# Kernel optimization log

Hardware: AMD Instinct MI355X
Metric: run time of the kernel (lower is better)

Reference implementation:

```python
import jax, jax.numpy as jnp
import numpy as np

N = 50000
E = 800000
NODE_F = 5
MAP_F = 32
EDGE_F = 4
HID = 64
RNN = 20
RNN_E = 8
LAT = 32
OUT = 4


def setup_inputs() -> dict:
    key = jax.random.key(0)
    ks = iter(jax.random.split(key, 40))
    def rn(shape, scale=0.1):
        return jax.random.normal(next(ks), shape, dtype=jnp.float32) * scale
    inp = {
        "x": rn((N, NODE_F), 1.0),
        "u": rn((N, MAP_F), 1.0),
        "edge_index": jax.random.randint(next(ks), (2, E), 0, N, dtype=jnp.int32),
        "edge_attr": rn((E, EDGE_F), 1.0),
        "h_node_h": rn((N, RNN), 1.0),
        "h_node_c": rn((N, RNN), 1.0),
        "h_edge_h": rn((N, RNN_E), 1.0),
        "h_edge_c": rn((N, RNN_E), 1.0),
        # node-history LSTM (input = node_features + map_encoding_size = 37)
        "W_ih_n": rn((4 * RNN, NODE_F + MAP_F)), "W_hh_n": rn((4 * RNN, RNN)),
        "b_ih_n": jnp.zeros((4 * RNN,), jnp.float32), "b_hh_n": jnp.zeros((4 * RNN,), jnp.float32),
        # edge-history LSTM (input = latent_edge_features)
        "W_ih_e": rn((4 * RNN_E, LAT)), "W_hh_e": rn((4 * RNN_E, RNN_E)),
        "b_ih_e": jnp.zeros((4 * RNN_E,), jnp.float32), "b_hh_e": jnp.zeros((4 * RNN_E,), jnp.float32),
        # message edge MLP: in = 2*37 + 4 = 78 -> 64 -> 32
        "We1": rn((2 * (NODE_F + MAP_F) + EDGE_F, HID)), "be1": jnp.zeros((HID,), jnp.float32),
        "We2": rn((HID, LAT)), "be2": jnp.zeros((LAT,), jnp.float32),
        # GN_out edge MLP: in = 2*(rnn_size + rnn_edge_size) + 4 = 60 -> 64 -> 32
        "Wo1": rn((2 * (RNN + RNN_E) + EDGE_F, HID)), "bo1": jnp.zeros((HID,), jnp.float32),
        "Wo2": rn((HID, LAT)), "bo2": jnp.zeros((LAT,), jnp.float32),
        # GN_out node MLP: in = (rnn_size + rnn_edge_size) + latent = 60 -> 64 -> 4
        "Wn1": rn((RNN + RNN_E + LAT, HID)), "bn1": jnp.zeros((HID,), jnp.float32),
        "Wn2": rn((HID, OUT)), "bn2": jnp.zeros((OUT,), jnp.float32),
    }
    return inp


def _lstm_step(xin, h, c, Wih, Whh, bih, bhh):
    # torch gate order: i, f, g, o
    g = xin @ Wih.T + h @ Whh.T + bih + bhh
    i, f, gg, o = jnp.split(g, 4, axis=-1)
    c_new = jax.nn.sigmoid(f) * c + jax.nn.sigmoid(i) * jnp.tanh(gg)
    h_new = jax.nn.sigmoid(o) * jnp.tanh(c_new)
    return h_new, c_new


def _segment_mean(vals, idx, n):
    s = jax.ops.segment_sum(vals, idx, num_segments=n)
    cnt = jax.ops.segment_sum(jnp.ones((vals.shape[0], 1), vals.dtype), idx, num_segments=n)
    return s / jnp.maximum(cnt, 1.0)


def _edge_mlp(src, dst, edge_attr, W1, b1, W2, b2):
    h = jnp.concatenate([src, dst, edge_attr], axis=-1)
    return jax.nn.relu(h @ W1 + b1) @ W2 + b2


def reference(x, u, edge_index, edge_attr, h_node_h, h_node_c, h_edge_h, h_edge_c,
              W_ih_n, W_hh_n, b_ih_n, b_hh_n, W_ih_e, W_hh_e, b_ih_e, b_hh_e,
              We1, be1, We2, be2, Wo1, bo1, Wo2, bo2, Wn1, bn1, Wn2, bn2):
    n = x.shape[0]
    xu = jnp.concatenate([x, u], axis=-1)  # [N, 37]
    # node history RNN step
    node_hist, node_c = _lstm_step(xu, h_node_h, h_node_c, W_ih_n, W_hh_n, b_ih_n, b_hh_n)
    # message GN: gather -> edge MLP
    row, col = edge_index[0], edge_index[1]
    messages = _edge_mlp(xu[row], xu[col], edge_attr, We1, be1, We2, be2)  # [E, 32]
    # edge history RNN: aggregate messages per receiving node, then LSTM step
    agg_msg = _segment_mean(messages, col, n)  # [N, 32]
    edge_hist, edge_c = _lstm_step(agg_msg, h_edge_h, h_edge_c, W_ih_e, W_hh_e, b_ih_e, b_hh_e)
    # output GN block
    full = jnp.concatenate([node_hist, edge_hist], axis=-1)  # [N, 28]
    e2 = _edge_mlp(full[row], full[col], edge_attr, Wo1, bo1, Wo2, bo2)  # [E, 32]
    agg2 = _segment_mean(e2, col, n)  # [N, 32]
    node_in = jnp.concatenate([full, agg2], axis=-1)  # [N, 60]
    out = jax.nn.relu(node_in @ Wn1 + bn1) @ Wn2 + bn2  # [N, 4]
    return (out, node_hist, node_c, edge_hist, edge_c)
```

## Files before the change

### kernel.cpp

```cpp
#include <hip/hip_runtime.h>
#include <math.h>

#define NN 50000
#define EE 800000
#define SBLK ((NN + 255) / 256)

typedef short bf16x8 __attribute__((ext_vector_type(8)));
typedef float f32x4 __attribute__((ext_vector_type(4)));
typedef unsigned short ushort_t;
#define MFMA16(a, b, c) __builtin_amdgcn_mfma_f32_16x16x32_bf16(a, b, c, 0, 0, 0)

__device__ __forceinline__ float sigmoidf_(float x) { return 1.0f / (1.0f + __expf(-x)); }

__device__ __forceinline__ unsigned short f2bf(float f) {
    unsigned u = __builtin_bit_cast(unsigned, f);
    u += 0x7FFFu + ((u >> 16) & 1u);
    return (unsigned short)(u >> 16);
}
__device__ __forceinline__ float bf2f(unsigned short v) {
    unsigned u = (unsigned)v << 16;
    return __builtin_bit_cast(float, u);
}
__device__ __forceinline__ unsigned pk2(float a, float b) {
    return ((unsigned)f2bf(b) << 16) | (unsigned)f2bf(a);
}

__global__ __launch_bounds__(256) void node_lstm_k(
    const float* __restrict__ x, const float* __restrict__ u,
    const float* __restrict__ h0, const float* __restrict__ c0,
    const float* __restrict__ Wih, const float* __restrict__ Whh,
    const float* __restrict__ bih, const float* __restrict__ bhh,
    ushort_t* __restrict__ xu16, float* __restrict__ h_out, float* __restrict__ c_out)
{
    __shared__ float sWih[80 * 37];
    __shared__ float sWhh[80 * 20];
    __shared__ float sb[80];
    for (int i = threadIdx.x; i < 80 * 37; i += 256) sWih[i] = Wih[i];
    for (int i = threadIdx.x; i < 80 * 20; i += 256) sWhh[i] = Whh[i];
    if (threadIdx.x < 80) sb[threadIdx.x] = bih[threadIdx.x] + bhh[threadIdx.x];
    __syncthreads();
    int n = blockIdx.x * 256 + threadIdx.x;
    if (n >= NN) return;

    float xu[40];
#pragma unroll
    for (int k = 0; k < 5; k++) xu[k] = x[n * 5 + k];
#pragma unroll
    for (int k = 0; k < 32; k++) xu[5 + k] = u[n * 32 + k];
    xu[37] = 0.f; xu[38] = 0.f; xu[39] = 0.f;

    {
        unsigned w[20];
#pragma unroll
        for (int k = 0; k < 20; k++) w[k] = pk2(xu[2 * k], xu[2 * k + 1]);
        uint4* dst = (uint4*)(xu16 + (size_t)n * 40);
#pragma unroll
        for (int q = 0; q < 5; q++)
            dst[q] = make_uint4(w[q * 4], w[q * 4 + 1], w[q * 4 + 2], w[q * 4 + 3]);
    }

    float h[20];
#pragma unroll
    for (int k = 0; k < 20; k++) h[k] = h0[n * 20 + k];

#pragma unroll 1
    for (int r = 0; r < 20; r++) {
        float gi = sb[r], gf = sb[20 + r], gg = sb[40 + r], go = sb[60 + r];
#pragma unroll
        for (int k = 0; k < 37; k++) {
            float v = xu[k];
            gi = fmaf(v, sWih[r * 37 + k], gi);
            gf = fmaf(v, sWih[(20 + r) * 37 + k], gf);
            gg = fmaf(v, sWih[(40 + r) * 37 + k], gg);
            go = fmaf(v, sWih[(60 + r) * 37 + k], go);
        }
#pragma unroll
        for (int k = 0; k < 20; k++) {
            float v = h[k];
            gi = fmaf(v, sWhh[r * 20 + k], gi);
            gf = fmaf(v, sWhh[(20 + r) * 20 + k], gf);
            gg = fmaf(v, sWhh[(40 + r) * 20 + k], gg);
            go = fmaf(v, sWhh[(60 + r) * 20 + k], go);
        }
        float cr = c0[n * 20 + r];
        float cn = sigmoidf_(gf) * cr + sigmoidf_(gi) * tanhf(gg);
        float hn = sigmoidf_(go) * tanhf(cn);
        h_out[n * 20 + r] = hn;
        c_out[n * 20 + r] = cn;
    }
}

__global__ __launch_bounds__(256) void csr_count_k(const int* __restrict__ col,
                                                   int* __restrict__ count)
{
    int e = blockIdx.x * 256 + threadIdx.x;
    if (e < EE) atomicAdd(&count[col[e]], 1);
}

__global__ __launch_bounds__(256) void scan1_k(const int* __restrict__ count,
                                               int* __restrict__ bsum)
{
    __shared__ int red[256];
    int t = threadIdx.x;
    int i = blockIdx.x * 256 + t;
    red[t] = (i < NN) ? count[i] : 0;
    __syncthreads();
#pragma unroll
    for (int d = 128; d > 0; d >>= 1) {
        if (t < d) red[t] += red[t + d];
        __syncthreads();
    }
    if (t == 0) bsum[blockIdx.x] = red[0];
}

__global__ __launch_bounds__(256) void scan2_k(const int* __restrict__ bsum,
                                               int* __restrict__ bpre)
{
    __shared__ int s[256];
    int t = threadIdx.x;
    int v = (t < SBLK) ? bsum[t] : 0;
    s[t] = v;
    __syncthreads();
#pragma unroll
    for (int d = 1; d < 256; d <<= 1) {
        int w = (t >= d) ? s[t - d] : 0;
        __syncthreads();
        s[t] += w;
        __syncthreads();
    }
    if (t < SBLK) bpre[t] = s[t] - v;
}

__global__ __launch_bounds__(256) void scan3_k(const int* __restrict__ count,
                                               const int* __restrict__ bpre,
                                               int* __restrict__ offset,
                                               float* __restrict__ cntf)
{
    __shared__ int s[256];
    int t = threadIdx.x;
    int i = blockIdx.x * 256 + t;
    int v = (i < NN) ? count[i] : 0;
    s[t] = v;
    __syncthreads();
#pragma unroll
    for (int d = 1; d < 256; d <<= 1) {
        int w = (t >= d) ? s[t - d] : 0;
        __syncthreads();
        s[t] += w;
        __syncthreads();
    }
    if (i < NN) {
        offset[i] = bpre[blockIdx.x] + s[t] - v;
        cntf[i] = (float)v;
    }
}

__global__ __launch_bounds__(256) void csr_fill3_k(const int* __restrict__ row,
                                                   const int* __restrict__ col,
                                                   const float* __restrict__ eattr,
                                                   const int* __restrict__ offset,
                                                   int* __restrict__ cursor,
                                                   int* __restrict__ rowp,
                                                   int* __restrict__ colp,
                                                   ushort_t* __restrict__ eap)
{
    int e = blockIdx.x * 256 + threadIdx.x;
    if (e >= EE) return;
    int c = col[e];
    int pos = atomicAdd(&cursor[c], 1);
    int slot = offset[c] + pos;
    rowp[slot] = row[e];
    colp[slot] = c;
    float4 ev = *(const float4*)&eattr[(size_t)e * 4];
    uint2 pk = make_uint2(pk2(ev.x, ev.y), pk2(ev.z, ev.w));
    *(uint2*)&eap[(size_t)slot * 4] = pk;
}

template <int F, int STRIDE, int INK>
__global__ __launch_bounds__(256, 4) void edge_mlp_fused_k(
    const ushort_t* __restrict__ feat,
    const int* __restrict__ rowp, const int* __restrict__ colp,
    const ushort_t* __restrict__ eap,
    const int* __restrict__ offset, const int* __restrict__ count,
    const float* __restrict__ W1, const float* __restrict__ b1,
    const float* __restrict__ W2, const float* __restrict__ b2,
    float* __restrict__ agg)
{
    constexpr int S1 = INK / 32;
    constexpr int W1ST = INK + 8;
    constexpr int C1ST = 72;
    constexpr int ABYTES = (64 * W1ST + 32 * C1ST + 4 * 32 * C1ST) * 2;
    constexpr int BBYTES = 32 * 257 * 4;
    constexpr int UBYTES = (ABYTES > BBYTES) ? ABYTES : BBYTES;

    __shared__ __align__(16) char ldsu[UBYTES];
    __shared__ int colLds[256];
    __shared__ unsigned char segStartA[256];
    __shared__ short segEndA[256];
    __shared__ int segCnt;

    ushort_t* sW1 = (ushort_t*)ldsu;
    ushort_t* sW2 = sW1 + 64 * W1ST;
    ushort_t* sC1 = sW2 + 32 * C1ST;
    float*    msgT = (float*)ldsu;

    const int tid = threadIdx.x;
    const int B0 = blockIdx.x * 256;
    if (tid == 0) segCnt = 0;
    colLds[tid] = colp[B0 + tid];

    for (int i = tid; i < 64 * INK; i += 256) {
        int nk = i >> 6, n = i & 63;
        int kp = 0; bool z = false;
        if (F == 37) {
            if (nk < 37) kp = nk;
            else if (nk < 40) z = true;
            else if (nk < 77) kp = nk - 3;
            else if (nk < 80) z = true;
            else if (nk < 84) kp = nk - 6;
            else z = true;
        } else {
            if (nk < 28) kp = nk;
            else if (nk < 32) z = true;
            else kp = nk - 4;
        }
        sW1[n * W1ST + nk] = z ? (ushort_t)0 : f2bf(W1[kp * 64 + n]);
    }
    for (int i = tid; i < 64 * 32; i += 256) {
        int k = i >> 5, n = i & 31;
        sW2[n * C1ST + k] = f2bf(W2[k * 32 + n]);
    }
    __syncthreads();

    {
        bool isStart = (tid == 0) || (colLds[tid] != colLds[tid - 1]);
        if (isStart) {
            int node = colLds[tid];
            int off = offset[node], cn = count[node];
            int e = off + cn - B0; if (e > 256) e = 256;
            bool fullseg = (off >= B0) && (off + cn <= B0 + 256);
            int j = atomicAdd(&segCnt, 1);
            segStartA[j] = (unsigned char)tid;
            segEndA[j] = (short)(fullseg ? -e : e);
        }
    }

    const int wave = tid >> 6, lane = tid & 63;
    const int lr = lane & 15, jb = lane >> 4;
    const size_t slotBase = (size_t)B0 + (size_t)wave * 64;
    const float4* b1v = (const float4*)b1;
    ushort_t* myC1 = sC1 + wave * 32 * C1ST;
    const float bb2_0 = b2[lr], bb2_1 = b2[16 + lr];

    f32x4 acc2a[2][2][2];

#pragma unroll
    for (int half = 0; half < 2; half++) {
        bf16x8 xf[2][S1];
#pragma unroll
        for (int ne2 = 0; ne2 < 2; ne2++) {
            size_t slot = slotBase + (size_t)(half * 2 + ne2) * 16 + lr;
            const ushort_t* xr = feat + (size_t)rowp[slot] * STRIDE;
            const ushort_t* xc = feat + (size_t)colLds[slot - B0] * STRIDE;
            const ushort_t* ea = eap + slot * 4;
            xf[ne2][0] = *(const bf16x8*)(xr + jb * 8);
            if (F == 37) {
                const ushort_t* p1 = (jb == 0) ? (xr + 32) : (xc + (jb - 1) * 8);
                xf[ne2][1] = *(const bf16x8*)p1;
                const ushort_t* p2 = (jb == 0) ? (xc + 24) : ((jb == 1) ? (xc + 32) : ea);
                bf16x8 v = *(const bf16x8*)p2;
                if (jb >= 2) { v[4] = 0; v[5] = 0; v[6] = 0; v[7] = 0; }
                if (jb == 3) { v[0] = 0; v[1] = 0; v[2] = 0; v[3] = 0; }
                xf[ne2][2] = v;
            } else {
                const ushort_t* pl = (jb < 3) ? (xc + jb * 8) : (xc + 24);
                uint2 lo = *(const uint2*)pl;
                const ushort_t* ph = (jb < 3) ? (pl + 4) : ea;
                uint2 hi = *(const uint2*)ph;
                uint4 cc = make_uint4(lo.x, lo.y, hi.x, hi.y);
                xf[ne2][1] = __builtin_bit_cast(bf16x8, cc);
            }
        }

        f32x4 acc1[4][2];
#pragma unroll
        for (int mh = 0; mh < 4; mh++) {
            float4 bv = b1v[mh * 4 + jb];
            f32x4 bi = {bv.x, bv.y, bv.z, bv.w};
            acc1[mh][0] = bi; acc1[mh][1] = bi;
        }
#pragma unroll
        for (int s = 0; s < S1; s++) {
#pragma unroll
            for (int mh = 0; mh < 4; mh++) {
                bf16x8 wf = *(const bf16x8*)&sW1[(mh * 16 + lr) * W1ST + s * 32 + jb * 8];
                acc1[mh][0] = MFMA16(wf, xf[0][s], acc1[mh][0]);
                acc1[mh][1] = MFMA16(wf, xf[1][s], acc1[mh][1]);
            }
        }

#pragma unroll
        for (int mh = 0; mh < 4; mh++) {
#pragma unroll
            for (int ne2 = 0; ne2 < 2; ne2++) {
                f32x4 a = acc1[mh][ne2];
                unsigned w0 = pk2(fmaxf(a[0], 0.f), fmaxf(a[1], 0.f));
                unsigned w1 = pk2(fmaxf(a[2], 0.f), fmaxf(a[3], 0.f));
                *(uint2*)&myC1[(ne2 * 16 + lr) * C1ST + mh * 16 + jb * 4] = make_uint2(w0, w1);
            }
        }

#pragma unroll
        for (int m = 0; m < 2; m++) {
            acc2a[half][m][0] = f32x4{bb2_0, bb2_0, bb2_0, bb2_0};
            acc2a[half][m][1] = f32x4{bb2_1, bb2_1, bb2_1, bb2_1};
        }
#pragma unroll
        for (int s2 = 0; s2 < 2; s2++) {
            bf16x8 w2f0 = *(const bf16x8*)&sW2[lr * C1ST + s2 * 32 + jb * 8];
            bf16x8 w2f1 = *(const bf16x8*)&sW2[(16 + lr) * C1ST + s2 * 32 + jb * 8];
#pragma unroll
            for (int m = 0; m < 2; m++) {
                bf16x8 a2 = *(const bf16x8*)&myC1[(m * 16 + lr) * C1ST + s2 * 32 + jb * 8];
                acc2a[half][m][0] = MFMA16(a2, w2f0, acc2a[half][m][0]);
                acc2a[half][m][1] = MFMA16(a2, w2f1, acc2a[half][m][1]);
            }
        }
    }

    __syncthreads();
#pragma unroll
    for (int half = 0; half < 2; half++) {
#pragma unroll
        for (int m = 0; m < 2; m++) {
            int row = wave * 64 + (half * 2 + m) * 16 + jb * 4;
#pragma unroll
            for (int n = 0; n < 2; n++) {
                f32x4 a = acc2a[half][m][n];
                float* dst = &msgT[(size_t)(n * 16 + lr) * 257 + row];
                dst[0] = a[0]; dst[1] = a[1]; dst[2] = a[2]; dst[3] = a[3];
            }
        }
    }
    __syncthreads();

    {
        int f = lane & 31;
        int h = lane >> 5;
        const float* mrow = msgT + (size_t)f * 257;
        int nseg = segCnt;
        for (int j = wave; j < nseg; j += 4) {
            int s = segStartA[j];
            int ev = segEndA[j];
            bool fullseg = ev < 0;
            int e = fullseg ? -ev : ev;
            int node = colLds[s];
            float sum = 0.f;
            for (int i = s + h; i < e; i += 2) sum += mrow[i];
            sum += __shfl_xor(sum, 32);
            if (lane < 32) {
                float* dst = &agg[(size_t)node * 32 + f];
                if (fullseg) *dst = sum;
                else atomicAdd(dst, sum);
            }
        }
    }
}

__global__ __launch_bounds__(256) void edge_lstm_k(
    const float* __restrict__ agg, const float* __restrict__ cnt,
    const float* __restrict__ h0, const float* __restrict__ c0,
    const float* __restrict__ Wih, const float* __restrict__ Whh,
    const float* __restrict__ bih, const float* __restrict__ bhh,
    const float* __restrict__ node_h,
    float* __restrict__ h_out, float* __restrict__ c_out, ushort_t* __restrict__ full16)
{
    __shared__ float sWih[32 * 32];
    __shared__ float sWhh[32 * 8];
    __shared__ float sb[32];
    for (int i = threadIdx.x; i < 32 * 32; i += 256) sWih[i] = Wih[i];
    for (int i = threadIdx.x; i < 32 * 8; i += 256) sWhh[i] = Whh[i];
    if (threadIdx.x < 32) sb[threadIdx.x] = bih[threadIdx.x] + bhh[threadIdx.x];
    __syncthreads();
    int n = blockIdx.x * 256 + threadIdx.x;
    if (n >= NN) return;

    float inv = 1.0f / fmaxf(cnt[n], 1.0f);
    float msg[32];
#pragma unroll
    for (int k = 0; k < 32; k++) msg[k] = agg[(size_t)n * 32 + k] * inv;
    float h[8];
#pragma unroll
    for (int k = 0; k < 8; k++) h[k] = h0[n * 8 + k];

    float fl[32];
#pragma unroll
    for (int k = 0; k < 20; k++) fl[k] = node_h[n * 20 + k];
    fl[28] = 0.f; fl[29] = 0.f; fl[30] = 0.f; fl[31] = 0.f;

#pragma unroll
    for (int r = 0; r < 8; r++) {
        float gi = sb[r], gf = sb[8 + r], gg = sb[16 + r], go = sb[24 + r];
#pragma unroll
        for (int k = 0; k < 32; k++) {
            float v = msg[k];
            gi = fmaf(v, sWih[r * 32 + k], gi);
            gf = fmaf(v, sWih[(8 + r) * 32 + k], gf);
            gg = fmaf(v, sWih[(16 + r) * 32 + k], gg);
            go = fmaf(v, sWih[(24 + r) * 32 + k], go);
        }
#pragma unroll
        for (int k = 0; k < 8; k++) {
            float v = h[k];
            gi = fmaf(v, sWhh[r * 8 + k], gi);
            gf = fmaf(v, sWhh[(8 + r) * 8 + k], gf);
            gg = fmaf(v, sWhh[(16 + r) * 8 + k], gg);
            go = fmaf(v, sWhh[(24 + r) * 8 + k], go);
        }
        float cr = c0[n * 8 + r];
        float cn = sigmoidf_(gf) * cr + sigmoidf_(gi) * tanhf(gg);
        float hn = sigmoidf_(go) * tanhf(cn);
        h_out[n * 8 + r] = hn;
        c_out[n * 8 + r] = cn;
        fl[20 + r] = hn;
    }
    unsigned w[16];
#pragma unroll
    for (int k = 0; k < 16; k++) w[k] = pk2(fl[2 * k], fl[2 * k + 1]);
    uint4* dst = (uint4*)(full16 + (size_t)n * 32);
#pragma unroll
    for (int q = 0; q < 4; q++)
        dst[q] = make_uint4(w[q * 4], w[q * 4 + 1], w[q * 4 + 2], w[q * 4 + 3]);
}

__global__ __launch_bounds__(256) void node_out_k(
    const ushort_t* __restrict__ full16, const float* __restrict__ agg2, const float* __restrict__ cnt,
    const float* __restrict__ W1, const float* __restrict__ b1,
    const float* __restrict__ W2, const float* __restrict__ b2,
    float* __restrict__ out)
{
    __shared__ __align__(16) float sW1[60 * 64];
    __shared__ __align__(16) float sW2[64 * 4];
    __shared__ float sb1[64];
    __shared__ float sb2[4];
    for (int i = threadIdx.x; i < 60 * 64; i += 256) sW1[i] = W1[i];
    for (int i = threadIdx.x; i < 64 * 4; i += 256) sW2[i] = W2[i];
    if (threadIdx.x < 64) sb1[threadIdx.x] = b1[threadIdx.x];
    if (threadIdx.x < 4) sb2[threadIdx.x] = b2[threadIdx.x];
    __syncthreads();
    int n = blockIdx.x * 256 + threadIdx.x;
    if (n >= NN) return;

    float in[60];
    const ushort_t* fr = full16 + (size_t)n * 32;
#pragma unroll
    for (int k = 0; k < 28; k++) in[k] = bf2f(fr[k]);
    float inv = 1.0f / fmaxf(cnt[n], 1.0f);
#pragma unroll
    for (int k = 0; k < 32; k++) in[28 + k] = agg2[(size_t)n * 32 + k] * inv;

    float o[4] = {sb2[0], sb2[1], sb2[2], sb2[3]};
#pragma unroll 1
    for (int j = 0; j < 64; j += 4) {
        float s[4] = {sb1[j], sb1[j + 1], sb1[j + 2], sb1[j + 3]};
#pragma unroll
        for (int k = 0; k < 60; k++) {
            float4 w = *(const float4*)&sW1[k * 64 + j];
            s[0] = fmaf(in[k], w.x, s[0]);
            s[1] = fmaf(in[k], w.y, s[1]);
            s[2] = fmaf(in[k], w.z, s[2]);
            s[3] = fmaf(in[k], w.w, s[3]);
        }
#pragma unroll
        for (int jj = 0; jj < 4; jj++) {
            float sv = fmaxf(s[jj], 0.0f);
            float4 w = *(const float4*)&sW2[(j + jj) * 4];
            o[0] = fmaf(sv, w.x, o[0]);
            o[1] = fmaf(sv, w.y, o[1]);
            o[2] = fmaf(sv, w.z, o[2]);
            o[3] = fmaf(sv, w.w, o[3]);
        }
    }
#pragma unroll
    for (int m = 0; m < 4; m++) out[n * 4 + m] = o[m];
}

template <int F, int STRIDE, bool DO_CNT>
__global__ __launch_bounds__(256) void edge_mlp_atomic_k(
    const ushort_t* __restrict__ feat,
    const int* __restrict__ row, const int* __restrict__ col,
    const float* __restrict__ eattr,
    const float* __restrict__ W1, const float* __restrict__ b1,
    const float* __restrict__ W2, const float* __restrict__ b2,
    float* __restrict__ agg, float* __restrict__ cnt)
{
    constexpr int IN = 2 * F + 4;
    __shared__ __align__(16) float sW1[IN * 64];
    __shared__ __align__(16) float sW2[64 * 32];
    __shared__ float sb1[64];
    __shared__ float sb2[32];
    for (int i = threadIdx.x; i < IN * 64; i += 256) sW1[i] = W1[i];
    for (int i = threadIdx.x; i < 64 * 32; i += 256) sW2[i] = W2[i];
    if (threadIdx.x < 64) sb1[threadIdx.x] = b1[threadIdx.x];
    if (threadIdx.x < 32) sb2[threadIdx.x] = b2[threadIdx.x];
    __syncthreads();
    int e = blockIdx.x * 256 + threadIdx.x;
    if (e >= EE) return;

    int r = row[e], c = col[e];
    float h[IN];
#pragma unroll
    for (int k = 0; k < F; k++) h[k] = bf2f(feat[(size_t)r * STRIDE + k]);
#pragma unroll
    for (int k = 0; k < F; k++) h[F + k] = bf2f(feat[(size_t)c * STRIDE + k]);
    float4 ev = *(const float4*)&eattr[(size_t)e * 4];
    h[2 * F] = ev.x; h[2 * F + 1] = ev.y; h[2 * F + 2] = ev.z; h[2 * F + 3] = ev.w;

    float out[32];
#pragma unroll
    for (int m = 0; m < 32; m++) out[m] = sb2[m];
#pragma unroll 1
    for (int j = 0; j < 64; j += 4) {
        float s[4] = {sb1[j], sb1[j + 1], sb1[j + 2], sb1[j + 3]};
#pragma unroll
        for (int k = 0; k < IN; k++) {
            float4 w = *(const float4*)&sW1[k * 64 + j];
            s[0] = fmaf(h[k], w.x, s[0]);
            s[1] = fmaf(h[k], w.y, s[1]);
            s[2] = fmaf(h[k], w.z, s[2]);
            s[3] = fmaf(h[k], w.w, s[3]);
        }
        s[0] = fmaxf(s[0], 0.f); s[1] = fmaxf(s[1], 0.f);
        s[2] = fmaxf(s[2], 0.f); s[3] = fmaxf(s[3], 0.f);
#pragma unroll
        for (int jj = 0; jj < 4; jj++) {
#pragma unroll
            for (int m = 0; m < 32; m += 4) {
                float4 w = *(const float4*)&sW2[(j + jj) * 32 + m];
                out[m]     = fmaf(s[jj], w.x, out[m]);
                out[m + 1] = fmaf(s[jj], w.y, out[m + 1]);
                out[m + 2] = fmaf(s[jj], w.z, out[m + 2]);
                out[m + 3] = fmaf(s[jj], w.w, out[m + 3]);
            }
        }
    }
    float* dst = &agg[(size_t)c * 32];
#pragma unroll
    for (int m = 0; m < 32; m++) atomicAdd(&dst[m], out[m]);
    if (DO_CNT) atomicAdd(&cnt[c], 1.0f);
}

extern "C" void kernel_launch(void* const* d_in, const int* in_sizes, int n_in,
                              void* d_out, int out_size, void* d_ws, size_t ws_size,
                              hipStream_t stream) {
    (void)in_sizes; (void)n_in; (void)out_size;
    const float* x      = (const float*)d_in[0];
    const float* u      = (const float*)d_in[1];
    const int*   ei     = (const int*)d_in[2];
    const float* eattr  = (const float*)d_in[3];
    const float* hn_h   = (const float*)d_in[4];
    const float* hn_c   = (const float*)d_in[5];
    const float* he_h   = (const float*)d_in[6];
    const float* he_c   = (const float*)d_in[7];
    const float* Wih_n  = (const float*)d_in[8];
    const float* Whh_n  = (const float*)d_in[9];
    const float* bih_n  = (const float*)d_in[10];
    const float* bhh_n  = (const float*)d_in[11];
    const float* Wih_e  = (const float*)d_in[12];
    const float* Whh_e  = (const float*)d_in[13];
    const float* bih_e  = (const float*)d_in[14];
    const float* bhh_e  = (const float*)d_in[15];
    const float* We1    = (const float*)d_in[16];
    const float* be1    = (const float*)d_in[17];
    const float* We2    = (const float*)d_in[18];
    const float* be2    = (const float*)d_in[19];
    const float* Wo1    = (const float*)d_in[20];
    const float* bo1    = (const float*)d_in[21];
    const float* Wo2    = (const float*)d_in[22];
    const float* bo2    = (const float*)d_in[23];
    const float* Wn1    = (const float*)d_in[24];
    const float* bn1    = (const float*)d_in[25];
    const float* Wn2    = (const float*)d_in[26];
    const float* bn2    = (const float*)d_in[27];

    const int* row = ei;
    const int* col = ei + EE;

    float* out = (float*)d_out;
    float* out_y   = out;
    float* node_h  = out + (size_t)NN * 4;
    float* node_c  = out + (size_t)NN * 24;
    float* edge_h  = out + (size_t)NN * 44;
    float* edge_c  = out + (size_t)NN * 52;

    int nb_n = (NN + 255) / 256;
    int nb_e = (EE + 255) / 256;

    ushort_t* xu16   = (ushort_t*)d_ws;
    ushort_t* full16 = xu16 + (size_t)NN * 40;
    float* agg  = (float*)(full16 + (size_t)NN * 32);
    float* cntf = agg + (size_t)NN * 32;
    float* agg2 = cntf + NN;
    int* count  = (int*)(agg2 + (size_t)NN * 32);
    int* cursor = count + NN;
    int* offset = cursor + NN;
    int* bsum   = offset + NN;
    int* bpre   = bsum + SBLK;
    int* rowp   = bpre + SBLK;
    int* colp   = rowp + EE;
    ushort_t* eap = (ushort_t*)(colp + EE);
    size_t needed = (size_t)((char*)(eap + (size_t)(EE + 4) * 4) - (char*)d_ws);

    if (ws_size >= needed) {
        hipMemsetAsync(agg, 0, (size_t)NN * (32 + 1 + 32 + 1 + 1) * sizeof(float), stream);

        node_lstm_k<<<nb_n, 256, 0, stream>>>(x, u, hn_h, hn_c, Wih_n, Whh_n, bih_n, bhh_n,
                                              xu16, node_h, node_c);
        csr_count_k<<<nb_e, 256, 0, stream>>>(col, count);
        scan1_k<<<SBLK, 256, 0, stream>>>(count, bsum);
        scan2_k<<<1, 256, 0, stream>>>(bsum, bpre);
        scan3_k<<<SBLK, 256, 0, stream>>>(count, bpre, offset, cntf);
        csr_fill3_k<<<nb_e, 256, 0, stream>>>(row, col, eattr, offset, cursor, rowp, colp, eap);

        edge_mlp_fused_k<37, 40, 96><<<EE / 256, 256, 0, stream>>>(
            xu16, rowp, colp, eap, offset, count, We1, be1, We2, be2, agg);
        edge_lstm_k<<<nb_n, 256, 0, stream>>>(agg, cntf, he_h, he_c, Wih_e, Whh_e, bih_e, bhh_e,
                                              node_h, edge_h, edge_c, full16);
        edge_mlp_fused_k<28, 32, 64><<<EE / 256, 256, 0, stream>>>(
            full16, rowp, colp, eap, offset, count, Wo1, bo1, Wo2, bo2, agg2);
        node_out_k<<<nb_n, 256, 0, stream>>>(full16, agg2, cntf, Wn1, bn1, Wn2, bn2, out_y);
    } else {
        hipMemsetAsync(agg, 0, (size_t)NN * (32 + 1 + 32) * sizeof(float), stream);
        node_lstm_k<<<nb_n, 256, 0, stream>>>(x, u, hn_h, hn_c, Wih_n, Whh_n, bih_n, bhh_n,
                                              xu16, node_h, node_c);
        edge_mlp_atomic_k<37, 40, true><<<nb_e, 256, 0, stream>>>(xu16, row, col, eattr,
                                                                  We1, be1, We2, be2, agg, cntf);
        edge_lstm_k<<<nb_n, 256, 0, stream>>>(agg, cntf, he_h, he_c, Wih_e, Whh_e, bih_e, bhh_e,
                                              node_h, edge_h, edge_c, full16);
        edge_mlp_atomic_k<28, 32, false><<<nb_e, 256, 0, stream>>>(full16, row, col, eattr,
                                                                   Wo1, bo1, Wo2, bo2, agg2, nullptr);
        node_out_k<<<nb_n, 256, 0, stream>>>(full16, agg2, cntf, Wn1, bn1, Wn2, bn2, out_y);
    }
}
```

Measured before the change: 289.4 us.

## Prepack bf16 MLP weights once and interleave CSR edge records into uint4

A new single-block kernel converts and pads the two edge-MLP weight sets to bf16 in their LDS layout once per call. Each edge-MLP block then fills shared memory with a plain vector copy instead of every block converting and transposing the fp32 weights. The CSR fill now writes row, col and the packed edge attributes as one 16-byte record, so the edge kernels read one coalesced uint4 per edge instead of three separate arrays. The cost is an extra tiny kernel launch and a little more padding bytes per edge.

```diff
diff --git a/kernel.cpp b/kernel.cpp
--- a/kernel.cpp
+++ b/kernel.cpp
@@ -23,6 +23,55 @@
 }
 __device__ __forceinline__ unsigned pk2(float a, float b) {
     return ((unsigned)f2bf(b) << 16) | (unsigned)f2bf(a);
+}
+
+#define W1ST_A 104
+#define W1ST_B 72
+#define C1ST_  72
+#define PW1A (64 * W1ST_A)
+#define PW2A (32 * C1ST_)
+#define PW1B (64 * W1ST_B)
+#define PW2B (32 * C1ST_)
+
+__global__ __launch_bounds__(256) void pack_w_k(
+    const float* __restrict__ We1, const float* __restrict__ We2,
+    const float* __restrict__ Wo1, const float* __restrict__ Wo2,
+    ushort_t* __restrict__ pw)
+{
+    ushort_t* pw1a = pw;
+    ushort_t* pw2a = pw1a + PW1A;
+    ushort_t* pw1b = pw2a + PW2A;
+    ushort_t* pw2b = pw1b + PW1B;
+    int tid = threadIdx.x;
+
+    for (int i = tid; i < PW1A; i += 256) {
+        int n = i / W1ST_A, nk = i - n * W1ST_A;
+        int kp = 0; bool z = false;
+        if (nk < 37) kp = nk;
+        else if (nk < 40) z = true;
+        else if (nk < 77) kp = nk - 3;
+        else if (nk < 80) z = true;
+        else if (nk < 84) kp = nk - 6;
+        else z = true;
+        pw1a[i] = z ? (ushort_t)0 : f2bf(We1[kp * 64 + n]);
+    }
+    for (int i = tid; i < PW2A; i += 256) {
+        int n = i / C1ST_, k = i - n * C1ST_;
+        pw2a[i] = (k < 64) ? f2bf(We2[k * 32 + n]) : (ushort_t)0;
+    }
+    for (int i = tid; i < PW1B; i += 256) {
+        int n = i / W1ST_B, nk = i - n * W1ST_B;
+        int kp = 0; bool z = false;
+        if (nk < 28) kp = nk;
+        else if (nk < 32) z = true;
+        else if (nk < 64) kp = nk - 4;
+        else z = true;
+        pw1b[i] = z ? (ushort_t)0 : f2bf(Wo1[kp * 64 + n]);
+    }
+    for (int i = tid; i < PW2B; i += 256) {
+        int n = i / C1ST_, k = i - n * C1ST_;
+        pw2b[i] = (k < 64) ? f2bf(Wo2[k * 32 + n]) : (ushort_t)0;
+    }
 }
 
 __global__ __launch_bounds__(256) void node_lstm_k(
@@ -155,43 +204,38 @@
     }
 }
 
-__global__ __launch_bounds__(256) void csr_fill3_k(const int* __restrict__ row,
+__global__ __launch_bounds__(256) void csr_fill4_k(const int* __restrict__ row,
                                                    const int* __restrict__ col,
                                                    const float* __restrict__ eattr,
                                                    const int* __restrict__ offset,
                                                    int* __restrict__ cursor,
-                                                   int* __restrict__ rowp,
-                                                   int* __restrict__ colp,
-                                                   ushort_t* __restrict__ eap)
+                                                   uint4* __restrict__ edat)
 {
     int e = blockIdx.x * 256 + threadIdx.x;
     if (e >= EE) return;
     int c = col[e];
     int pos = atomicAdd(&cursor[c], 1);
     int slot = offset[c] + pos;
-    rowp[slot] = row[e];
-    colp[slot] = c;
     float4 ev = *(const float4*)&eattr[(size_t)e * 4];
-    uint2 pk = make_uint2(pk2(ev.x, ev.y), pk2(ev.z, ev.w));
-    *(uint2*)&eap[(size_t)slot * 4] = pk;
+    edat[slot] = make_uint4((unsigned)row[e], (unsigned)c, pk2(ev.x, ev.y), pk2(ev.z, ev.w));
 }
 
 template <int F, int STRIDE, int INK>
 __global__ __launch_bounds__(256, 4) void edge_mlp_fused_k(
     const ushort_t* __restrict__ feat,
-    const int* __restrict__ rowp, const int* __restrict__ colp,
-    const ushort_t* __restrict__ eap,
+    const uint4* __restrict__ edat,
     const int* __restrict__ offset, const int* __restrict__ count,
-    const float* __restrict__ W1, const float* __restrict__ b1,
-    const float* __restrict__ W2, const float* __restrict__ b2,
+    const ushort_t* __restrict__ pw,
+    const float* __restrict__ b1, const float* __restrict__ b2,
     float* __restrict__ agg)
 {
     constexpr int S1 = INK / 32;
     constexpr int W1ST = INK + 8;
-    constexpr int C1ST = 72;
+    constexpr int C1ST = C1ST_;
     constexpr int ABYTES = (64 * W1ST + 32 * C1ST + 4 * 32 * C1ST) * 2;
     constexpr int BBYTES = 32 * 257 * 4;
     constexpr int UBYTES = (ABYTES > BBYTES) ? ABYTES : BBYTES;
+    constexpr int NU4 = (64 * W1ST + 32 * C1ST) / 8;
 
     __shared__ __align__(16) char ldsu[UBYTES];
     __shared__ int colLds[256];
@@ -207,28 +251,12 @@
     const int tid = threadIdx.x;
     const int B0 = blockIdx.x * 256;
     if (tid == 0) segCnt = 0;
-    colLds[tid] = colp[B0 + tid];
-
-    for (int i = tid; i < 64 * INK; i += 256) {
-        int nk = i >> 6, n = i & 63;
-        int kp = 0; bool z = false;
-        if (F == 37) {
-            if (nk < 37) kp = nk;
-            else if (nk < 40) z = true;
-            else if (nk < 77) kp = nk - 3;
-            else if (nk < 80) z = true;
-            else if (nk < 84) kp = nk - 6;
-            else z = true;
-        } else {
-            if (nk < 28) kp = nk;
-            else if (nk < 32) z = true;
-            else kp = nk - 4;
-        }
-        sW1[n * W1ST + nk] = z ? (ushort_t)0 : f2bf(W1[kp * 64 + n]);
-    }
-    for (int i = tid; i < 64 * 32; i += 256) {
-        int k = i >> 5, n = i & 31;
-        sW2[n * C1ST + k] = f2bf(W2[k * 32 + n]);
+    colLds[tid] = (int)edat[B0 + tid].y;
+
+    {
+        const uint4* src = (const uint4*)pw;
+        uint4* dst = (uint4*)ldsu;
+        for (int i = tid; i < NU4; i += 256) dst[i] = src[i];
     }
     __syncthreads();
 
@@ -260,25 +288,32 @@
 #pragma unroll
         for (int ne2 = 0; ne2 < 2; ne2++) {
             size_t slot = slotBase + (size_t)(half * 2 + ne2) * 16 + lr;
-            const ushort_t* xr = feat + (size_t)rowp[slot] * STRIDE;
-            const ushort_t* xc = feat + (size_t)colLds[slot - B0] * STRIDE;
-            const ushort_t* ea = eap + slot * 4;
+            uint4 ed = edat[slot];
+            const ushort_t* xr = feat + (size_t)ed.x * STRIDE;
+            const ushort_t* xc = feat + (size_t)ed.y * STRIDE;
             xf[ne2][0] = *(const bf16x8*)(xr + jb * 8);
             if (F == 37) {
                 const ushort_t* p1 = (jb == 0) ? (xr + 32) : (xc + (jb - 1) * 8);
                 xf[ne2][1] = *(const bf16x8*)p1;
-                const ushort_t* p2 = (jb == 0) ? (xc + 24) : ((jb == 1) ? (xc + 32) : ea);
-                bf16x8 v = *(const bf16x8*)p2;
-                if (jb >= 2) { v[4] = 0; v[5] = 0; v[6] = 0; v[7] = 0; }
-                if (jb == 3) { v[0] = 0; v[1] = 0; v[2] = 0; v[3] = 0; }
+                bf16x8 v;
+                if (jb < 2) {
+                    v = *(const bf16x8*)((jb == 0) ? (xc + 24) : (xc + 32));
+                } else if (jb == 2) {
+                    uint4 t = make_uint4(ed.z, ed.w, 0u, 0u);
+                    v = __builtin_bit_cast(bf16x8, t);
+                } else {
+                    uint4 t = make_uint4(0u, 0u, 0u, 0u);
+                    v = __builtin_bit_cast(bf16x8, t);
+                }
                 xf[ne2][2] = v;
             } else {
-                const ushort_t* pl = (jb < 3) ? (xc + jb * 8) : (xc + 24);
-                uint2 lo = *(const uint2*)pl;
-                const ushort_t* ph = (jb < 3) ? (pl + 4) : ea;
-                uint2 hi = *(const uint2*)ph;
-                uint4 cc = make_uint4(lo.x, lo.y, hi.x, hi.y);
-                xf[ne2][1] = __builtin_bit_cast(bf16x8, cc);
+                if (jb < 3) {
+                    xf[ne2][1] = *(const bf16x8*)(xc + jb * 8);
+                } else {
+                    uint2 lo = *(const uint2*)(xc + 24);
+                    uint4 t = make_uint4(lo.x, lo.y, ed.z, ed.w);
+                    xf[ne2][1] = __builtin_bit_cast(bf16x8, t);
+                }
             }
         }
 
@@ -606,28 +641,30 @@
     int* offset = cursor + NN;
     int* bsum   = offset + NN;
     int* bpre   = bsum + SBLK;
-    int* rowp   = bpre + SBLK;
-    int* colp   = rowp + EE;
-    ushort_t* eap = (ushort_t*)(colp + EE);
-    size_t needed = (size_t)((char*)(eap + (size_t)(EE + 4) * 4) - (char*)d_ws);
+    size_t pw_off = ((size_t)((char*)(bpre + SBLK) - (char*)d_ws) + 15) & ~(size_t)15;
+    ushort_t* pw = (ushort_t*)((char*)d_ws + pw_off);
+    size_t edat_off = ((pw_off + (size_t)(PW1A + PW2A + PW1B + PW2B) * 2) + 15) & ~(size_t)15;
+    uint4* edat = (uint4*)((char*)d_ws + edat_off);
+    size_t needed = edat_off + (size_t)EE * 16;
 
     if (ws_size >= needed) {
         hipMemsetAsync(agg, 0, (size_t)NN * (32 + 1 + 32 + 1 + 1) * sizeof(float), stream);
 
+        pack_w_k<<<1, 256, 0, stream>>>(We1, We2, Wo1, Wo2, pw);
         node_lstm_k<<<nb_n, 256, 0, stream>>>(x, u, hn_h, hn_c, Wih_n, Whh_n, bih_n, bhh_n,
                                               xu16, node_h, node_c);
         csr_count_k<<<nb_e, 256, 0, stream>>>(col, count);
         scan1_k<<<SBLK, 256, 0, stream>>>(count, bsum);
         scan2_k<<<1, 256, 0, stream>>>(bsum, bpre);
         scan3_k<<<SBLK, 256, 0, stream>>>(count, bpre, offset, cntf);
-        csr_fill3_k<<<nb_e, 256, 0, stream>>>(row, col, eattr, offset, cursor, rowp, colp, eap);
+        csr_fill4_k<<<nb_e, 256, 0, stream>>>(row, col, eattr, offset, cursor, edat);
 
         edge_mlp_fused_k<37, 40, 96><<<EE / 256, 256, 0, stream>>>(
-            xu16, rowp, colp, eap, offset, count, We1, be1, We2, be2, agg);
+            xu16, edat, offset, count, pw, be1, be2, agg);
         edge_lstm_k<<<nb_n, 256, 0, stream>>>(agg, cntf, he_h, he_c, Wih_e, Whh_e, bih_e, bhh_e,
                                               node_h, edge_h, edge_c, full16);
         edge_mlp_fused_k<28, 32, 64><<<EE / 256, 256, 0, stream>>>(
-            full16, rowp, colp, eap, offset, count, Wo1, bo1, Wo2, bo2, agg2);
+            full16, edat, offset, count, pw + PW1A + PW2A, bo1, bo2, agg2);
         node_out_k<<<nb_n, 256, 0, stream>>>(full16, agg2, cntf, Wn1, bn1, Wn2, bn2, out_y);
     } else {
         hipMemsetAsync(agg, 0, (size_t)NN * (32 + 1 + 32) * sizeof(float), stream);
```

After: 261.5 us. 1.11x faster.
